# Optimization experiments

Hardware: AMD Instinct MI355X
Metric: run time of the kernel (lower is better)

Reference implementation:

```python
import jax, jax.numpy as jnp
import numpy as np

B, L, D = 4, 2048, 1024
H = 16
HD = D // H  # head_dim = 64
BASE = 10000.0


def rope_cos_sin(seq_len, head_dim, dtype=jnp.float32):
    inv_freq = 1.0 / (BASE ** (jnp.arange(0, head_dim, 2, dtype=jnp.float32) / head_dim))
    t = jnp.arange(seq_len, dtype=jnp.float32)
    freqs = jnp.outer(t, inv_freq)  # [L, HD/2]
    return jnp.cos(freqs).astype(dtype), jnp.sin(freqs).astype(dtype)


def apply_rope(x, cos, sin):
    # x: [B, H, L, HD]; cos/sin: [L, HD/2]
    x1 = x[..., ::2]
    x2 = x[..., 1::2]
    c = cos[None, None, :, :]
    s = sin[None, None, :, :]
    # NOTE: original concatenates halves (does not re-interleave)
    return jnp.concatenate([x1 * c - x2 * s, x1 * s + x2 * c], axis=-1)


def setup_inputs() -> dict:
    key = jax.random.key(0)
    k1, k2, k3 = jax.random.split(key, 3)
    x = jax.random.normal(k1, (B, L, D), dtype=jnp.float32)
    W_qkv = jax.random.normal(k2, (3 * D, D), dtype=jnp.float32) * (D ** -0.5)
    W_proj = jax.random.normal(k3, (D, D), dtype=jnp.float32) * (D ** -0.5)
    return {"x": x, "W_qkv": W_qkv, "W_proj": W_proj}


def reference(x, W_qkv, W_proj):
    b, l, d = x.shape
    scale = HD ** -0.5
    qkv = jnp.einsum('bld,ed->ble', x, W_qkv)            # [B, L, 3D]
    qkv = qkv.reshape(b, l, 3, H, HD)
    q, k, v = (jnp.transpose(qkv[:, :, i], (0, 2, 1, 3)) for i in range(3))  # [B,H,L,HD]
    cos, sin = rope_cos_sin(l, HD, x.dtype)
    q = apply_rope(q, cos, sin)
    k = apply_rope(k, cos, sin)
    attn = jnp.einsum('bhqd,bhkd->bhqk', q, k) * scale   # [B,H,L,L]
    attn = jax.nn.softmax(attn, axis=-1)
    out = jnp.einsum('bhqk,bhkd->bhqd', attn, v)         # [B,H,L,HD]
    out = jnp.transpose(out, (0, 2, 1, 3)).reshape(b, l, d)
    return jnp.einsum('bld,ed->ble', out, W_proj)
```

## Files before the change

kernel.cpp:

```cpp
#include <hip/hip_runtime.h>
#include <hip/hip_bf16.h>

typedef unsigned short u16;
typedef unsigned int u32;
typedef __attribute__((ext_vector_type(8))) short bf16x8;
typedef __attribute__((ext_vector_type(4))) float f32x4;

#define NB 4
#define NL 2048
#define ND 1024
#define NH 16

__device__ __forceinline__ float bf2f(u16 v) {
    union { float f; unsigned u; } x; x.u = ((unsigned)v) << 16; return x.f;
}
__device__ __forceinline__ u16 f2bf(float f) {
    union { __hip_bfloat16 h; u16 u; } x; x.h = __float2bfloat16(f); return x.u;
}
__device__ __forceinline__ u32 pk2(float a, float b) {
    union { float f; u32 u; } x, y; x.f = a; y.f = b;
    return ((x.u + 0x8000u) >> 16) | ((y.u + 0x8000u) & 0xffff0000u);
}
#if __has_builtin(__builtin_amdgcn_exp2f)
#define EXP2F(x) __builtin_amdgcn_exp2f(x)
#else
#define EXP2F(x) __expf((x) * 0.69314718056f)
#endif

__device__ __forceinline__ void gload_lds16(const u16* g, u16* l) {
    __builtin_amdgcn_global_load_lds(
        (__attribute__((address_space(1))) void*)(g),
        (__attribute__((address_space(3))) void*)(l), 16, 0, 0);
}

__global__ __launch_bounds__(256) void cast_k(const float* __restrict__ in,
                                              u16* __restrict__ out, int n4) {
    int i = blockIdx.x * 256 + threadIdx.x;
    if (i >= n4) return;
    float4 v = *(const float4*)&in[i * 4];
    u16 tmp[4] = {f2bf(v.x), f2bf(v.y), f2bf(v.z), f2bf(v.w)};
    *(ushort4*)&out[i * 4] = *(ushort4*)tmp;
}

__global__ __launch_bounds__(256) void rope_table_k(float* __restrict__ cosT,
                                                    float* __restrict__ sinT) {
    int idx = blockIdx.x * 256 + threadIdx.x;
    int l = idx >> 5, i = idx & 31;
    double invf = pow(10000.0, -((double)(2 * i)) / 64.0);
    double ang = (double)l * invf;
    cosT[idx] = (float)cos(ang);
    sinT[idx] = (float)sin(ang);
}

template <typename OutT>
__global__ __launch_bounds__(256) void gemm_bt(const u16* __restrict__ A,
                                               const u16* __restrict__ Bm,
                                               OutT* __restrict__ C,
                                               int M, int N, int K) {
    __shared__ u16 As[128][64];
    __shared__ u16 Bs[128][64];
    const int t = threadIdx.x;
    const int lane = t & 63, wave = t >> 6;
    const int quad = lane >> 4, lrow = lane & 15;
    const int wr = wave >> 1, wc = wave & 1;
    const size_t m0 = (size_t)blockIdx.y * 128, n0 = (size_t)blockIdx.x * 128;

    const int srow = wave * 32 + (lane >> 3);
    const int scg  = (lane & 7) ^ (lane >> 3);

    f32x4 acc[4][4];
#pragma unroll
    for (int i = 0; i < 4; ++i)
#pragma unroll
        for (int j = 0; j < 4; ++j) acc[i][j] = (f32x4)0.0f;

    for (int k0 = 0; k0 < K; k0 += 64) {
#pragma unroll
        for (int j = 0; j < 4; ++j) {
            gload_lds16(&A[(m0 + srow + j * 8) * K + k0 + scg * 8],
                        &As[wave * 32 + j * 8][0]);
            gload_lds16(&Bm[(n0 + srow + j * 8) * K + k0 + scg * 8],
                        &Bs[wave * 32 + j * 8][0]);
        }
        __syncthreads();
#pragma unroll
        for (int ks = 0; ks < 2; ++ks) {
            bf16x8 av[4], bv[4];
#pragma unroll
            for (int i = 0; i < 4; ++i)
                av[i] = *(const bf16x8*)
                    &As[wr * 64 + i * 16 + lrow][(((ks << 2) | quad) ^ (lrow & 7)) << 3];
#pragma unroll
            for (int j = 0; j < 4; ++j)
                bv[j] = *(const bf16x8*)
                    &Bs[wc * 64 + j * 16 + lrow][(((ks << 2) | quad) ^ (lrow & 7)) << 3];
#pragma unroll
            for (int i = 0; i < 4; ++i)
#pragma unroll
                for (int j = 0; j < 4; ++j)
                    acc[i][j] = __builtin_amdgcn_mfma_f32_16x16x32_bf16(
                        av[i], bv[j], acc[i][j], 0, 0, 0);
        }
        __syncthreads();
    }
#pragma unroll
    for (int i = 0; i < 4; ++i)
#pragma unroll
        for (int r = 0; r < 4; ++r) {
            size_t row = m0 + wr * 64 + i * 16 + quad * 4 + r;
#pragma unroll
            for (int j = 0; j < 4; ++j) {
                size_t col = n0 + wc * 64 + j * 16 + lrow;
                if constexpr (sizeof(OutT) == 4)
                    C[row * N + col] = acc[i][j][r];
                else
                    C[row * N + col] = f2bf(acc[i][j][r]);
            }
        }
}

__global__ __launch_bounds__(1024) void rope_qk_k(const u16* __restrict__ qkv,
                                                  const float* __restrict__ cosT,
                                                  const float* __restrict__ sinT,
                                                  u16* __restrict__ Q,
                                                  u16* __restrict__ Ko) {
    const int row = blockIdx.x;
    const int l = row & (NL - 1);
    const int b = row >> 11;
    const int t = threadIdx.x;
    const int h = t >> 6, d = t & 63;
    const int i = d & 31;
    const float c = cosT[l * 32 + i], s = sinT[l * 32 + i];
    const u16* base = qkv + (size_t)row * 3072;
    float q0 = bf2f(base[h * 64 + 2 * i]);
    float q1 = bf2f(base[h * 64 + 2 * i + 1]);
    float k0 = bf2f(base[1024 + h * 64 + 2 * i]);
    float k1 = bf2f(base[1024 + h * 64 + 2 * i + 1]);
    float qo = (d < 32) ? (q0 * c - q1 * s) : (q0 * s + q1 * c);
    float ko = (d < 32) ? (k0 * c - k1 * s) : (k0 * s + k1 * c);
    size_t oi = ((size_t)(b * NH + h) * NL + l) * 64 + d;
    Q[oi] = f2bf(qo * 0.180336879f);
    Ko[oi] = f2bf(ko);
}

__global__ __launch_bounds__(256) void vt_k(const u16* __restrict__ qkv,
                                            u16* __restrict__ VT) {
    __shared__ u16 tile[64][72];
    const int lt = blockIdx.x;
    const int bh = blockIdx.y;
    const int b = bh >> 4, h = bh & 15;
    const int l0 = lt * 64;
    const int t = threadIdx.x;
#pragma unroll
    for (int c = 0; c < 2; ++c) {
        int flat8 = t * 2 + c;
        int li = flat8 >> 3, dg = flat8 & 7;
        *(uint4*)&tile[li][dg * 8] =
            *(const uint4*)&qkv[((size_t)(b * NL + l0 + li)) * 3072 + 2048 + h * 64 + dg * 8];
    }
    __syncthreads();
#pragma unroll
    for (int c = 0; c < 2; ++c) {
        int flat8 = t * 2 + c;
        int d = flat8 >> 3, lg = flat8 & 7;
        u16 tmp[8];
#pragma unroll
        for (int e = 0; e < 8; ++e) tmp[e] = tile[lg * 8 + e][d];
        *(uint4*)&VT[((size_t)(bh * 64 + d)) * NL + l0 + lg * 8] = *(uint4*)tmp;
    }
}

__global__ __launch_bounds__(256) void attn_k(const u16* __restrict__ Q,
                                              const u16* __restrict__ Kg,
                                              const u16* __restrict__ VT,
                                              u16* __restrict__ Og) {
    __shared__ __align__(16) char smem[33792];
    u16 (*Qs)[64]  = (u16(*)[64])(smem);
    u16 (*Ks)[64]  = (u16(*)[64])(smem + 8192);
    u16 (*VsT)[64] = (u16(*)[64])(smem + 16384);
    const int t = threadIdx.x;
    const int lane = t & 63, wave = t >> 6;
    const int quad = lane >> 4, lq = lane & 15;
    u16 (*Ps)[72] = (u16(*)[72])(smem + 24576 + wave * 2304);

    const int qt = blockIdx.x, bh = blockIdx.y;
    const int q0 = qt * 64;
    const size_t qkbase = (size_t)bh * NL * 64;

    const int rloc = wave * 16 + (lane >> 3);
    const int scg  = (lane & 7) ^ (lane >> 3);

#pragma unroll
    for (int j = 0; j < 2; ++j)
        gload_lds16(&Q[qkbase + (size_t)(q0 + rloc + j * 8) * 64 + scg * 8],
                    &Qs[wave * 16 + j * 8][0]);

    const bf16x8 ones = (bf16x8)(short)16256;
    f32x4 ot[4];
#pragma unroll
    for (int mt = 0; mt < 4; ++mt) ot[mt] = (f32x4)0.0f;
    f32x4 lacc = (f32x4)0.0f;

    for (int kc = 0; kc < NL / 64; ++kc) {
        const int kb = kc * 64;
        __syncthreads();
#pragma unroll
        for (int j = 0; j < 2; ++j) {
            gload_lds16(&Kg[qkbase + (size_t)(kb + rloc + j * 8) * 64 + scg * 8],
                        &Ks[wave * 16 + j * 8][0]);
            gload_lds16(&VT[qkbase + (size_t)(rloc + j * 8) * NL + kb + scg * 8],
                        &VsT[wave * 16 + j * 8][0]);
        }
        __syncthreads();

        f32x4 st[4];
#pragma unroll
        for (int mt = 0; mt < 4; ++mt) st[mt] = (f32x4)0.0f;
#pragma unroll
        for (int ks = 0; ks < 2; ++ks) {
            bf16x8 bq = *(const bf16x8*)
                &Qs[wave * 16 + lq][(((ks << 2) | quad) ^ (lq & 7)) << 3];
#pragma unroll
            for (int mt = 0; mt < 4; ++mt) {
                bf16x8 ak = *(const bf16x8*)
                    &Ks[mt * 16 + lq][(((ks << 2) | quad) ^ (lq & 7)) << 3];
                st[mt] = __builtin_amdgcn_mfma_f32_16x16x32_bf16(ak, bq, st[mt], 0, 0, 0);
            }
        }

#pragma unroll
        for (int mt = 0; mt < 4; ++mt) {
            float p0 = EXP2F(st[mt][0]), p1 = EXP2F(st[mt][1]);
            float p2 = EXP2F(st[mt][2]), p3 = EXP2F(st[mt][3]);
            *(uint2*)&Ps[lq][mt * 16 + quad * 4] = make_uint2(pk2(p0, p1), pk2(p2, p3));
        }
        __builtin_amdgcn_s_waitcnt(0xc07f);

#pragma unroll
        for (int ks = 0; ks < 2; ++ks) {
            bf16x8 bp = *(const bf16x8*)&Ps[lq][ks * 32 + quad * 8];
            lacc = __builtin_amdgcn_mfma_f32_16x16x32_bf16(ones, bp, lacc, 0, 0, 0);
#pragma unroll
            for (int mt = 0; mt < 4; ++mt) {
                bf16x8 av = *(const bf16x8*)
                    &VsT[mt * 16 + lq][(((ks << 2) | quad) ^ (lq & 7)) << 3];
                ot[mt] = __builtin_amdgcn_mfma_f32_16x16x32_bf16(av, bp, ot[mt], 0, 0, 0);
            }
        }
    }

    __syncthreads();
    float* OT_ls = (float*)(smem + wave * 4352);
    float* Ls_ls = (float*)(smem + 17408);
#pragma unroll
    for (int mt = 0; mt < 4; ++mt)
#pragma unroll
        for (int r = 0; r < 4; ++r)
            OT_ls[(mt * 16 + quad * 4 + r) * 17 + lq] = ot[mt][r];
    if (quad == 0) Ls_ls[wave * 16 + lq] = lacc[0];
    __builtin_amdgcn_s_waitcnt(0xc07f);

    const int qq = lane >> 2, dblk = lane & 3;
    float rls = 1.0f / Ls_ls[wave * 16 + qq];
    u16 tmp[16];
#pragma unroll
    for (int e = 0; e < 16; ++e)
        tmp[e] = f2bf(OT_ls[(dblk * 16 + e) * 17 + qq] * rls);
    const int b = bh >> 4, h = bh & 15;
    size_t orow = (size_t)b * NL + q0 + wave * 16 + qq;
    size_t obase = orow * 1024 + h * 64 + dblk * 16;
    *(uint4*)&Og[obase] = *(uint4*)&tmp[0];
    *(uint4*)&Og[obase + 8] = *(uint4*)&tmp[8];
}

extern "C" void kernel_launch(void* const* d_in, const int* in_sizes, int n_in,
                              void* d_out, int out_size, void* d_ws, size_t ws_size,
                              hipStream_t stream) {
    const float* x     = (const float*)d_in[0];
    const float* Wqkv  = (const float*)d_in[1];
    const float* Wproj = (const float*)d_in[2];
    float* out = (float*)d_out;

    char* ws = (char*)d_ws;
    u16* qkv     = (u16*)ws;
    u16* attnout = (u16*)ws;
    u16* Qw      = (u16*)(ws + 50331648);
    u16* Kw      = (u16*)(ws + 67108864);
    u16* VTw     = (u16*)(ws + 83886080);
    float* cosT  = (float*)(ws + 100663296);
    float* sinT  = (float*)(ws + 100925440);
    u16* x_bf    = (u16*)(ws + 101187584);
    u16* Wqkv_bf = (u16*)(ws + 117964800);
    u16* Wproj_bf= (u16*)(ws + 124256256);

    rope_table_k<<<256, 256, 0, stream>>>(cosT, sinT);
    cast_k<<<8192, 256, 0, stream>>>(x, x_bf, 2097152);
    cast_k<<<3072, 256, 0, stream>>>(Wqkv, Wqkv_bf, 786432);
    cast_k<<<1024, 256, 0, stream>>>(Wproj, Wproj_bf, 262144);
    gemm_bt<u16><<<dim3(24, 64), 256, 0, stream>>>(x_bf, Wqkv_bf, qkv, 8192, 3072, 1024);
    rope_qk_k<<<8192, 1024, 0, stream>>>(qkv, cosT, sinT, Qw, Kw);
    vt_k<<<dim3(32, 64), 256, 0, stream>>>(qkv, VTw);
    attn_k<<<dim3(32, 64), 256, 0, stream>>>(Qw, Kw, VTw, attnout);
    gemm_bt<float><<<dim3(8, 64), 256, 0, stream>>>(attnout, Wproj_bf, out, 8192, 1024, 1024);
}
```

Before: 318.8 us.

## Double attention query tile to 8 waves sharing K/V loads; vectorize RoPE

The attention kernel now processes 128 query rows per block with 512 threads, so each K/V chunk staged in shared memory serves twice as many queries. Each wave loads half as much per chunk and uses incrementing pointers. Probabilities are packed to bf16 by truncation via a byte-permute instead of rounding. The RoPE kernel now handles four elements per thread with vector loads and stores, with the softmax scale folded into cos/sin. The larger block raises LDS use per block and may lower occupancy. Truncation adds a small bias to P.

```diff
diff --git a/kernel.cpp b/kernel.cpp
--- a/kernel.cpp
+++ b/kernel.cpp
@@ -20,6 +20,10 @@
 __device__ __forceinline__ u32 pk2(float a, float b) {
     union { float f; u32 u; } x, y; x.f = a; y.f = b;
     return ((x.u + 0x8000u) >> 16) | ((y.u + 0x8000u) & 0xffff0000u);
+}
+__device__ __forceinline__ u32 pkt(float lo, float hi) {
+    union { float f; u32 u; } x, y; x.f = lo; y.f = hi;
+    return __builtin_amdgcn_perm(y.u, x.u, 0x07060302u);
 }
 #if __has_builtin(__builtin_amdgcn_exp2f)
 #define EXP2F(x) __builtin_amdgcn_exp2f(x)
@@ -119,28 +123,38 @@
         }
 }
 
-__global__ __launch_bounds__(1024) void rope_qk_k(const u16* __restrict__ qkv,
-                                                  const float* __restrict__ cosT,
-                                                  const float* __restrict__ sinT,
-                                                  u16* __restrict__ Q,
-                                                  u16* __restrict__ Ko) {
+__global__ __launch_bounds__(256) void rope_qk_k(const u16* __restrict__ qkv,
+                                                 const float* __restrict__ cosT,
+                                                 const float* __restrict__ sinT,
+                                                 u16* __restrict__ Q,
+                                                 u16* __restrict__ Ko) {
     const int row = blockIdx.x;
     const int l = row & (NL - 1);
     const int b = row >> 11;
     const int t = threadIdx.x;
-    const int h = t >> 6, d = t & 63;
-    const int i = d & 31;
-    const float c = cosT[l * 32 + i], s = sinT[l * 32 + i];
-    const u16* base = qkv + (size_t)row * 3072;
-    float q0 = bf2f(base[h * 64 + 2 * i]);
-    float q1 = bf2f(base[h * 64 + 2 * i + 1]);
-    float k0 = bf2f(base[1024 + h * 64 + 2 * i]);
-    float k1 = bf2f(base[1024 + h * 64 + 2 * i + 1]);
-    float qo = (d < 32) ? (q0 * c - q1 * s) : (q0 * s + q1 * c);
-    float ko = (d < 32) ? (k0 * c - k1 * s) : (k0 * s + k1 * c);
-    size_t oi = ((size_t)(b * NH + h) * NL + l) * 64 + d;
-    Q[oi] = f2bf(qo * 0.180336879f);
-    Ko[oi] = f2bf(ko);
+    const int h = t >> 4, sub = t & 15;
+    const u16* base = qkv + (size_t)row * 3072 + h * 64 + sub * 4;
+    uint2 qv = *(const uint2*)base;
+    uint2 kv = *(const uint2*)(base + 1024);
+    float2 c2 = *(const float2*)&cosT[l * 32 + sub * 2];
+    float2 s2 = *(const float2*)&sinT[l * 32 + sub * 2];
+    union { float f; u32 u; } w;
+    float q0, q1, q2, q3, k0, k1, k2, k3;
+    w.u = qv.x << 16; q0 = w.f; w.u = qv.x & 0xffff0000u; q1 = w.f;
+    w.u = qv.y << 16; q2 = w.f; w.u = qv.y & 0xffff0000u; q3 = w.f;
+    w.u = kv.x << 16; k0 = w.f; w.u = kv.x & 0xffff0000u; k1 = w.f;
+    w.u = kv.y << 16; k2 = w.f; w.u = kv.y & 0xffff0000u; k3 = w.f;
+    const float SC = 0.180336879f;
+    float cq0 = c2.x * SC, sq0 = s2.x * SC, cq1 = c2.y * SC, sq1 = s2.y * SC;
+    u32 qlo = pk2(q0 * cq0 - q1 * sq0, q2 * cq1 - q3 * sq1);
+    u32 qhi = pk2(q0 * sq0 + q1 * cq0, q2 * sq1 + q3 * cq1);
+    u32 klo = pk2(k0 * c2.x - k1 * s2.x, k2 * c2.y - k3 * s2.y);
+    u32 khi = pk2(k0 * s2.x + k1 * c2.x, k2 * s2.y + k3 * c2.y);
+    size_t ob = ((size_t)(b * NH + h) * NL + l) * 64;
+    *(u32*)&Q[ob + sub * 2] = qlo;
+    *(u32*)&Q[ob + sub * 2 + 32] = qhi;
+    *(u32*)&Ko[ob + sub * 2] = klo;
+    *(u32*)&Ko[ob + sub * 2 + 32] = khi;
 }
 
 __global__ __launch_bounds__(256) void vt_k(const u16* __restrict__ qkv,
@@ -170,30 +184,33 @@
     }
 }
 
-__global__ __launch_bounds__(256) void attn_k(const u16* __restrict__ Q,
+__global__ __launch_bounds__(512) void attn_k(const u16* __restrict__ Q,
                                               const u16* __restrict__ Kg,
                                               const u16* __restrict__ VT,
                                               u16* __restrict__ Og) {
-    __shared__ __align__(16) char smem[33792];
+    __shared__ __align__(16) char smem[51200];
     u16 (*Qs)[64]  = (u16(*)[64])(smem);
-    u16 (*Ks)[64]  = (u16(*)[64])(smem + 8192);
-    u16 (*VsT)[64] = (u16(*)[64])(smem + 16384);
+    u16 (*Ks)[64]  = (u16(*)[64])(smem + 16384);
+    u16 (*VsT)[64] = (u16(*)[64])(smem + 24576);
     const int t = threadIdx.x;
     const int lane = t & 63, wave = t >> 6;
     const int quad = lane >> 4, lq = lane & 15;
-    u16 (*Ps)[72] = (u16(*)[72])(smem + 24576 + wave * 2304);
+    u16 (*Ps)[72] = (u16(*)[72])(smem + 32768 + wave * 2304);
 
     const int qt = blockIdx.x, bh = blockIdx.y;
-    const int q0 = qt * 64;
+    const int q0 = qt * 128;
     const size_t qkbase = (size_t)bh * NL * 64;
 
-    const int rloc = wave * 16 + (lane >> 3);
-    const int scg  = (lane & 7) ^ (lane >> 3);
+    const int rsub = lane >> 3;
+    const int scg  = (lane & 7) ^ rsub;
 
 #pragma unroll
     for (int j = 0; j < 2; ++j)
-        gload_lds16(&Q[qkbase + (size_t)(q0 + rloc + j * 8) * 64 + scg * 8],
+        gload_lds16(&Q[qkbase + (size_t)(q0 + wave * 16 + j * 8 + rsub) * 64 + scg * 8],
                     &Qs[wave * 16 + j * 8][0]);
+
+    const u16* kptr = Kg + qkbase + (size_t)(wave * 8 + rsub) * 64 + scg * 8;
+    const u16* vptr = VT + qkbase + (size_t)(wave * 8 + rsub) * NL + scg * 8;
 
     const bf16x8 ones = (bf16x8)(short)16256;
     f32x4 ot[4];
@@ -202,15 +219,11 @@
     f32x4 lacc = (f32x4)0.0f;
 
     for (int kc = 0; kc < NL / 64; ++kc) {
-        const int kb = kc * 64;
         __syncthreads();
-#pragma unroll
-        for (int j = 0; j < 2; ++j) {
-            gload_lds16(&Kg[qkbase + (size_t)(kb + rloc + j * 8) * 64 + scg * 8],
-                        &Ks[wave * 16 + j * 8][0]);
-            gload_lds16(&VT[qkbase + (size_t)(rloc + j * 8) * NL + kb + scg * 8],
-                        &VsT[wave * 16 + j * 8][0]);
-        }
+        gload_lds16(kptr, &Ks[wave * 8][0]);
+        gload_lds16(vptr, &VsT[wave * 8][0]);
+        kptr += 64 * 64;
+        vptr += 64;
         __syncthreads();
 
         f32x4 st[4];
@@ -230,9 +243,9 @@
 
 #pragma unroll
         for (int mt = 0; mt < 4; ++mt) {
-            float p0 = EXP2F(st[mt][0]), p1 = EXP2F(st[mt][1]);
-            float p2 = EXP2F(st[mt][2]), p3 = EXP2F(st[mt][3]);
-            *(uint2*)&Ps[lq][mt * 16 + quad * 4] = make_uint2(pk2(p0, p1), pk2(p2, p3));
+            *(uint2*)&Ps[lq][mt * 16 + quad * 4] =
+                make_uint2(pkt(EXP2F(st[mt][0]), EXP2F(st[mt][1])),
+                           pkt(EXP2F(st[mt][2]), EXP2F(st[mt][3])));
         }
         __builtin_amdgcn_s_waitcnt(0xc07f);
 
@@ -251,7 +264,7 @@
 
     __syncthreads();
     float* OT_ls = (float*)(smem + wave * 4352);
-    float* Ls_ls = (float*)(smem + 17408);
+    float* Ls_ls = (float*)(smem + 34816);
 #pragma unroll
     for (int mt = 0; mt < 4; ++mt)
 #pragma unroll
@@ -298,8 +311,8 @@
     cast_k<<<3072, 256, 0, stream>>>(Wqkv, Wqkv_bf, 786432);
     cast_k<<<1024, 256, 0, stream>>>(Wproj, Wproj_bf, 262144);
     gemm_bt<u16><<<dim3(24, 64), 256, 0, stream>>>(x_bf, Wqkv_bf, qkv, 8192, 3072, 1024);
-    rope_qk_k<<<8192, 1024, 0, stream>>>(qkv, cosT, sinT, Qw, Kw);
+    rope_qk_k<<<8192, 256, 0, stream>>>(qkv, cosT, sinT, Qw, Kw);
     vt_k<<<dim3(32, 64), 256, 0, stream>>>(qkv, VTw);
-    attn_k<<<dim3(32, 64), 256, 0, stream>>>(Qw, Kw, VTw, attnout);
+    attn_k<<<dim3(16, 64), 512, 0, stream>>>(Qw, Kw, VTw, attnout);
     gemm_bt<float><<<dim3(8, 64), 256, 0, stream>>>(attnout, Wproj_bf, out, 8192, 1024, 1024);
 }
```

After: 293.6 us. 7.9% less time.
